# Kernel optimization log

Measured on AMD Instinct MI355X. Metric: run time of the kernel, lower is better.

The kernel has to match this reference:

```python
import jax, jax.numpy as jnp
import numpy as np

NOPE, ROPE, LORA, VDIM = 128, 64, 512, 128
H, T = 16, 2048
SCALE = 1.0 / float(np.sqrt(NOPE + ROPE))  # 192**-0.5


def setup_inputs() -> dict:
    key = jax.random.key(0)
    k1, k2, k3, k4, k5 = jax.random.split(key, 5)
    return {
        "query": jax.random.normal(k1, (T, H, NOPE + ROPE), jnp.float32),
        "k_c_normed": jax.random.normal(k2, (T, LORA), jnp.float32),
        "k_pe": jax.random.normal(k3, (T, ROPE), jnp.float32),
        "w_kv_b": jax.random.normal(k4, (LORA, H * (NOPE + VDIM)), jnp.float32) * 0.02,
        "w_uv": jax.random.normal(k5, (H, LORA, VDIM), jnp.float32) * 0.02,
    }


def reference(query, k_c_normed, k_pe, w_kv_b, w_uv):
    # Causal (fresh-token, "compute friendly") MLA path of HPUUnifiedMLAImpl.
    t = query.shape[0]
    # kv_b_proj: latent -> per-head [nope | v]; only k_nope is used for scoring
    kv_nope = (k_c_normed @ w_kv_b).reshape(t, H, NOPE + VDIM)
    k_nope = kv_nope[..., :NOPE]                                   # [T,H,128]
    # k = cat(k_nope, broadcast k_pe) -> [T,H,192]
    k = jnp.concatenate(
        [k_nope, jnp.broadcast_to(k_pe[:, None, :], (t, H, ROPE))], axis=-1)
    # causal attention scores [H,T,T]
    scores = jnp.einsum('thd,shd->hts', query, k) * SCALE
    mask = jnp.tril(jnp.ones((t, t), dtype=bool))                  # causal
    scores = jnp.where(mask[None], scores, jnp.finfo(scores.dtype).min)
    p = jax.nn.softmax(scores, axis=-1)
    # value is the latent k_c, shared across heads (v_causal_latent expand)
    out_latent = jnp.einsum('hts,sl->thl', p, k_c_normed)          # [T,H,512]
    # W_UV projects latent attn output -> full v dim
    out = jnp.einsum('thl,hlv->thv', out_latent, w_uv)             # [T,H,128]
    return out.reshape(t, H * VDIM)
```

## Files before the change

### kernel.cpp

```cpp
#include <hip/hip_runtime.h>
#include <hip/hip_bf16.h>
#include <math.h>

#define T_SEQ 2048
#define NHEAD 16
#define DQK 192
#define DNOPE 128
#define DROPE 64
#define LORA_D 512
#define VDIM 128
#define SCALE_F 0.072168783648703216f
#define KC 32

typedef short bf16x8 __attribute__((ext_vector_type(8)));
typedef float f32x4 __attribute__((ext_vector_type(4)));

static __device__ __forceinline__ unsigned short f2bf(float x) {
  union { float f; unsigned int u; } v; v.f = x;
  unsigned int r = (v.u + 0x7fff + ((v.u >> 16) & 1)) >> 16;
  return (unsigned short)r;
}

__global__ __launch_bounds__(256) void stage_all(
    const float* __restrict__ k_c, const float* __restrict__ w_kv_b,
    const float* __restrict__ w_uv, unsigned short* __restrict__ Ab,
    unsigned short* __restrict__ BkT, unsigned short* __restrict__ BvT)
{
  __shared__ float tile[32][33];
  const int bx = blockIdx.x, role = blockIdx.y;
  const int tid = threadIdx.x;
  if (role == 0) {
    int i = (bx * 256 + tid) * 4;
    float4 v = *(const float4*)(k_c + i);
    ushort4 o = {f2bf(v.x), f2bf(v.y), f2bf(v.z), f2bf(v.w)};
    *(ushort4*)(Ab + i) = o;
    return;
  }
  const int tk = tid >> 3, tc4 = (tid & 7) * 4;
  const int wr = tid >> 3, wk4 = (tid & 7) * 4;
  if (role == 1) {
    const int k0 = (bx & 15) * 32, n0 = (bx >> 4) * 32;
    int n = n0 + tc4;
    int col = n + ((n >> 7) << 7);
    float4 v = *(const float4*)&w_kv_b[(size_t)(k0 + tk) * 4096 + col];
    tile[tk][tc4 + 0] = v.x; tile[tk][tc4 + 1] = v.y;
    tile[tk][tc4 + 2] = v.z; tile[tk][tc4 + 3] = v.w;
    __syncthreads();
    ushort4 o = {f2bf(tile[wk4 + 0][wr]), f2bf(tile[wk4 + 1][wr]),
                 f2bf(tile[wk4 + 2][wr]), f2bf(tile[wk4 + 3][wr])};
    *(ushort4*)&BkT[(size_t)(n0 + wr) * LORA_D + k0 + wk4] = o;
  } else {
    const int k0 = (bx & 15) * 32, v0 = ((bx >> 4) & 3) * 32, h = bx >> 6;
    float4 v = *(const float4*)&w_uv[(size_t)h * 65536 + (size_t)(k0 + tk) * 128 + v0 + tc4];
    tile[tk][tc4 + 0] = v.x; tile[tk][tc4 + 1] = v.y;
    tile[tk][tc4 + 2] = v.z; tile[tk][tc4 + 3] = v.w;
    __syncthreads();
    ushort4 o = {f2bf(tile[wk4 + 0][wr]), f2bf(tile[wk4 + 1][wr]),
                 f2bf(tile[wk4 + 2][wr]), f2bf(tile[wk4 + 3][wr])};
    *(ushort4*)&BvT[(size_t)(h * VDIM + v0 + wr) * LORA_D + k0 + wk4] = o;
  }
}

__global__ __launch_bounds__(256) void prep_gemm(
    const unsigned short* __restrict__ A, const unsigned short* __restrict__ BkT,
    const unsigned short* __restrict__ BvT, const float* __restrict__ k_pe,
    unsigned short* __restrict__ Kb, unsigned short* __restrict__ Vt)
{
  __shared__ unsigned short SMEM[32768];
  const int m0 = blockIdx.x * 128;
  const int by = blockIdx.y;
  const int isK = (by < 16);
  const int n0 = (isK ? by : (by - 16)) * 128;
  const unsigned short* BT = isK ? BkT : BvT;
  const int tid = threadIdx.x;
  const int wid = tid >> 6, lane = tid & 63;
  const int l16 = lane & 15, quad = lane >> 4;
  const int wm = (wid >> 1) * 64, wn = (wid & 1) * 64;

  auto stage_pg = [&](int b, int k0) {
    const char* Asrc = (const char*)(A + (size_t)m0 * LORA_D + k0);
    const char* Bsrc = (const char*)(BT + (size_t)n0 * LORA_D + k0);
    char* Adst = (char*)SMEM + b * 16384;
    char* Bdst = (char*)SMEM + 32768 + b * 16384;
#pragma unroll
    for (int i = 0; i < 4; ++i) {
      int d = tid * 16 + i * 4096;
      int row = d >> 7, c = d & 127;
      int sc = c ^ ((row & 7) << 4);
      __builtin_amdgcn_global_load_lds(
          (const unsigned int*)(Asrc + (size_t)row * 1024 + sc),
          (unsigned int*)(Adst + d), 16, 0, 0);
      __builtin_amdgcn_global_load_lds(
          (const unsigned int*)(Bsrc + (size_t)row * 1024 + sc),
          (unsigned int*)(Bdst + d), 16, 0, 0);
    }
  };

  f32x4 acc[4][4];
#pragma unroll
  for (int i = 0; i < 4; ++i)
#pragma unroll
    for (int j = 0; j < 4; ++j) acc[i][j] = (f32x4){0.f, 0.f, 0.f, 0.f};

  stage_pg(0, 0);
  __syncthreads();
  for (int kc = 0; kc < 8; ++kc) {
    const int cur = kc & 1;
    if (kc < 7) stage_pg(cur ^ 1, (kc + 1) * 64);
#pragma unroll
    for (int kk = 0; kk < 2; ++kk) {
      bf16x8 af[4], bfr[4];
#pragma unroll
      for (int t = 0; t < 4; ++t) {
        int ra = wm + t * 16 + l16;
        af[t] = *(const bf16x8*)((char*)SMEM + cur * 16384 + ra * 128 +
                                 (((kk * 4 + quad) ^ (ra & 7)) << 4));
        int rb = wn + t * 16 + l16;
        bfr[t] = *(const bf16x8*)((char*)SMEM + 32768 + cur * 16384 + rb * 128 +
                                  (((kk * 4 + quad) ^ (rb & 7)) << 4));
      }
#pragma unroll
      for (int mt = 0; mt < 4; ++mt)
#pragma unroll
        for (int nt = 0; nt < 4; ++nt)
          acc[mt][nt] = __builtin_amdgcn_mfma_f32_16x16x32_bf16(af[mt], bfr[nt], acc[mt][nt], 0, 0, 0);
    }
    __syncthreads();
  }

  unsigned short* E = SMEM;
  if (isK) {
#pragma unroll
    for (int mt = 0; mt < 4; ++mt)
#pragma unroll
      for (int nt = 0; nt < 4; ++nt) {
        int ml = wm + mt * 16 + quad * 4;
        int d = wn + nt * 16 + l16;
#pragma unroll
        for (int r = 0; r < 4; ++r)
          E[(ml + r) * 136 + d] = f2bf(acc[mt][nt][r]);
      }
  } else {
#pragma unroll
    for (int mt = 0; mt < 4; ++mt)
#pragma unroll
      for (int nt = 0; nt < 4; ++nt) {
        int ml = wm + mt * 16 + quad * 4;
        int nl = wn + nt * 16 + l16;
#pragma unroll
        for (int r = 0; r < 4; ++r)
          E[nl * 136 + ml + r] = f2bf(acc[mt][nt][r]);
      }
  }
  __syncthreads();

  if (isK) {
    const int h = by;
#pragma unroll
    for (int i = 0; i < 8; ++i) {
      int idx = (i * 256 + tid) * 8;
      int row = idx >> 7, col = idx & 127;
      uint4 v = *(const uint4*)&E[row * 136 + col];
      *(uint4*)&Kb[(size_t)h * (T_SEQ * DQK) + (size_t)(m0 + row) * DQK + col] = v;
    }
    for (int e = tid; e < 128 * 16; e += 256) {
      int row = e >> 4, c4 = (e & 15) * 4;
      float4 v = *(const float4*)&k_pe[(size_t)(m0 + row) * DROPE + c4];
      ushort4 o = {f2bf(v.x), f2bf(v.y), f2bf(v.z), f2bf(v.w)};
      *(ushort4*)&Kb[(size_t)h * (T_SEQ * DQK) + (size_t)(m0 + row) * DQK + DNOPE + c4] = o;
    }
  } else {
#pragma unroll
    for (int i = 0; i < 8; ++i) {
      int idx = (i * 256 + tid) * 8;
      int row = idx >> 7, col = idx & 127;
      uint4 v = *(const uint4*)&E[row * 136 + col];
      *(uint4*)&Vt[(size_t)(n0 + row) * T_SEQ + m0 + col] = v;
    }
  }
}

__global__ __launch_bounds__(256, 4) void flash_mfma(
    const float* __restrict__ Q, const unsigned short* __restrict__ K,
    const unsigned short* __restrict__ Vt, float* __restrict__ outp,
    float* __restrict__ Opart, float* __restrict__ Lpart, int adaptive)
{
  __shared__ unsigned short SM[2 * KC * DQK];
  __shared__ unsigned short Vsm[2 * VDIM * KC];
  const int id = blockIdx.x;
  const int h = ((id & 7) << 1) | ((id >> 3) & 1);
  int q0, c0, c1, slot, direct;
  if (adaptive) {
    const int b = 79 - (id >> 4);
    int j, sp, s;
    if (b < 8)       { j = b;               sp = 0;            s = 1; }
    else if (b < 24) { j = 8 + (b - 8) / 2; sp = (b - 8) % 2;  s = 2; }
    else if (b < 48) { j = 16 + (b - 24) / 3; sp = (b - 24) % 3; s = 3; }
    else             { j = 24 + (b - 48) / 4; sp = (b - 48) % 4; s = 4; }
    q0 = j * 64;
    const int n = 2 * j + 2;
    c0 = (n * sp) / s;
    c1 = (n * (sp + 1)) / s;
    direct = (s == 1);
    slot = h * 72 + (b - 8);
  } else {
    q0 = (31 - (id >> 4)) * 64;
    c0 = 0; c1 = q0 / KC + 2; direct = 1; slot = 0;
  }
  const int tid = threadIdx.x;
  const int wid = tid >> 6;
  const int lane = tid & 63;
  const int l16 = lane & 15;
  const int quad = lane >> 4;
  const int myrow = q0 + wid * 16 + quad * 4;
  const int qrow  = q0 + wid * 16 + l16;
  const int nch = c1 - c0;

  const unsigned short* Kh = K + (size_t)h * T_SEQ * DQK;
  const unsigned short* Vth = Vt + (size_t)h * VDIM * T_SEQ;

  int ksrc_off[3], kdst_off[3];
#pragma unroll
  for (int i = 0; i < 3; ++i) {
    int d = tid * 16 + i * 4096;
    int rho = d / 384, c = d - rho * 384;
    int rr = rho & 15, hi = rho >> 4;
    int g = 8 * (rr >> 2) + 2 * (rr & 3) + hi;
    ksrc_off[i] = g * 384 + (c ^ ((rho & 7) << 4));
    kdst_off[i] = d;
  }
  size_t vsrc_off[2]; int vdst_off[2];
#pragma unroll
  for (int i = 0; i < 2; ++i) {
    int d = tid * 16 + i * 4096;
    int row = d >> 6, c = d & 63;
    vsrc_off[i] = (size_t)row * (T_SEQ * 2) + (c ^ ((row & 3) << 4));
    vdst_off[i] = d;
  }

  auto stage = [&](int buf, int s0) {
    const char* Kc = (const char*)Kh + (size_t)s0 * 384;
    char* Kd = (char*)&SM[buf * (KC * DQK)];
#pragma unroll
    for (int i = 0; i < 3; ++i)
      __builtin_amdgcn_global_load_lds(
          (const unsigned int*)(Kc + ksrc_off[i]),
          (unsigned int*)(Kd + kdst_off[i]), 16, 0, 0);
    const char* Vc = (const char*)Vth + (size_t)s0 * 2;
    char* Vd = (char*)&Vsm[buf * (VDIM * KC)];
#pragma unroll
    for (int i = 0; i < 2; ++i)
      __builtin_amdgcn_global_load_lds(
          (const unsigned int*)(Vc + vsrc_off[i]),
          (unsigned int*)(Vd + vdst_off[i]), 16, 0, 0);
  };

  for (int e = tid; e < 64 * 48; e += 256) {
    int row = e / 48, col = (e % 48) * 4;
    float4 q4 = *(const float4*)&Q[(size_t)(q0 + row) * (NHEAD * DQK) + h * DQK + col];
    ushort4 qp = {f2bf(q4.x), f2bf(q4.y), f2bf(q4.z), f2bf(q4.w)};
    *(ushort4*)&SM[row * DQK + col] = qp;
  }
  __syncthreads();
  bf16x8 qf[6];
#pragma unroll
  for (int ks = 0; ks < 6; ++ks)
    qf[ks] = *(const bf16x8*)&SM[(wid * 16 + l16) * DQK + ks * 32 + quad * 8];
  __syncthreads();
  stage(0, c0 * KC);
  __syncthreads();

  f32x4 oacc[8];
#pragma unroll
  for (int i = 0; i < 8; ++i) oacc[i] = (f32x4){0.f, 0.f, 0.f, 0.f};
  float lsum = 0.f;

  for (int ck = 0; ck < nch; ++ck) {
    const int cur = ck & 1;
    const int s0 = (c0 + ck) * KC;
    if (ck + 1 < nch) stage(cur ^ 1, s0 + KC);

    const char* Kbase = (const char*)&SM[cur * (KC * DQK)];
    f32x4 sacc0 = (f32x4){0.f, 0.f, 0.f, 0.f};
    f32x4 sacc1 = (f32x4){0.f, 0.f, 0.f, 0.f};
    __builtin_amdgcn_s_setprio(1);
#pragma unroll
    for (int ks = 0; ks < 6; ++ks) {
      int c = ks * 64 + quad * 16;
      int r0 = l16, r1 = 16 + l16;
      bf16x8 kf0 = *(const bf16x8*)(Kbase + r0 * 384 + (c ^ ((r0 & 7) << 4)));
      bf16x8 kf1 = *(const bf16x8*)(Kbase + r1 * 384 + (c ^ ((r1 & 7) << 4)));
      sacc0 = __builtin_amdgcn_mfma_f32_16x16x32_bf16(kf0, qf[ks], sacc0, 0, 0, 0);
      sacc1 = __builtin_amdgcn_mfma_f32_16x16x32_bf16(kf1, qf[ks], sacc1, 0, 0, 0);
    }
    __builtin_amdgcn_s_setprio(0);

    union { unsigned int u[4]; bf16x8 v; } pw;
#pragma unroll
    for (int r = 0; r < 4; ++r) {
      int kva = s0 + quad * 8 + 2 * r;
      float e0 = (kva <= qrow)     ? __expf(sacc0[r] * SCALE_F) : 0.f;
      float e1 = (kva + 1 <= qrow) ? __expf(sacc1[r] * SCALE_F) : 0.f;
      lsum += e0 + e1;
      asm("v_cvt_pk_bf16_f32 %0, %1, %2" : "=v"(pw.u[r]) : "v"(e0), "v"(e1));
    }
    bf16x8 pf = pw.v;

    const char* Vbase = (const char*)&Vsm[cur * (VDIM * KC)];
    __builtin_amdgcn_s_setprio(1);
#pragma unroll
    for (int nt = 0; nt < 8; ++nt) {
      int vrow = nt * 16 + l16;
      bf16x8 vf = *(const bf16x8*)(Vbase + vrow * 64 + ((quad * 16) ^ ((vrow & 3) << 4)));
      oacc[nt] = __builtin_amdgcn_mfma_f32_16x16x32_bf16(pf, vf, oacc[nt], 0, 0, 0);
    }
    __builtin_amdgcn_s_setprio(0);

    __syncthreads();
  }

  lsum += __shfl_xor(lsum, 16);
  lsum += __shfl_xor(lsum, 32);
  float rowsum[4];
#pragma unroll
  for (int r = 0; r < 4; ++r) rowsum[r] = __shfl(lsum, quad * 4 + r, 64);

  if (direct) {
    float inv[4];
#pragma unroll
    for (int r = 0; r < 4; ++r) inv[r] = 1.f / rowsum[r];
#pragma unroll
    for (int nt = 0; nt < 8; ++nt)
#pragma unroll
      for (int r = 0; r < 4; ++r)
        outp[(size_t)(myrow + r) * (NHEAD * VDIM) + h * VDIM + nt * 16 + l16] =
            oacc[nt][r] * inv[r];
  } else {
    const int rbase = wid * 16 + quad * 4;
#pragma unroll
    for (int nt = 0; nt < 8; ++nt)
#pragma unroll
      for (int r = 0; r < 4; ++r)
        Opart[(size_t)slot * 8192 + (rbase + r) * 128 + nt * 16 + l16] =
            oacc[nt][r];
    if (l16 == 0)
#pragma unroll
      for (int r = 0; r < 4; ++r)
        Lpart[slot * 64 + rbase + r] = rowsum[r];
  }
}

__global__ __launch_bounds__(256) void reduce_out(
    const float* __restrict__ Opart, const float* __restrict__ Lpart,
    float* __restrict__ outp)
{
  const int t = blockIdx.x;
  const int h = t & 15;
  const int j = 8 + (t >> 4);
  int s, b0;
  if (j < 16)      { s = 2; b0 = 8 + (j - 8) * 2; }
  else if (j < 24) { s = 3; b0 = 24 + (j - 16) * 3; }
  else             { s = 4; b0 = 48 + (j - 24) * 4; }
  const int slot = h * 72 + (b0 - 8);
  const int q0 = j * 64;
  const int tid = threadIdx.x;
#pragma unroll
  for (int i = 0; i < 8; ++i) {
    const int f4 = tid + i * 256;
    const int row = f4 >> 5, cc = f4 & 31;
    float ax = 0.f, ay = 0.f, az = 0.f, aw = 0.f, l = 0.f;
    for (int k = 0; k < s; ++k) {
      float4 v = ((const float4*)Opart)[(size_t)(slot + k) * 2048 + f4];
      ax += v.x; ay += v.y; az += v.z; aw += v.w;
      l += Lpart[(slot + k) * 64 + row];
    }
    const float inv = 1.f / l;
    float4 o = {ax * inv, ay * inv, az * inv, aw * inv};
    ((float4*)outp)[(size_t)(q0 + row) * 512 + h * 32 + cc] = o;
  }
}

extern "C" void kernel_launch(void* const* d_in, const int* in_sizes, int n_in,
                              void* d_out, int out_size, void* d_ws, size_t ws_size,
                              hipStream_t stream) {
  const float* query  = (const float*)d_in[0];
  const float* k_c    = (const float*)d_in[1];
  const float* k_pe   = (const float*)d_in[2];
  const float* w_kv_b = (const float*)d_in[3];
  const float* w_uv   = (const float*)d_in[4];
  float* outp = (float*)d_out;

  unsigned short* Kb  = (unsigned short*)d_ws;
  unsigned short* Vt  = Kb + (size_t)NHEAD * T_SEQ * DQK;
  unsigned short* Ab  = Vt + (size_t)NHEAD * VDIM * T_SEQ;
  unsigned short* BkT = Ab + (size_t)T_SEQ * LORA_D;
  unsigned short* BvT = BkT + (size_t)2048 * LORA_D;
  float* Opart = (float*)(BvT + (size_t)2048 * LORA_D);
  float* Lpart = Opart + (size_t)16 * 72 * 64 * 128;
  const size_t need =
      (size_t)((char*)(Lpart + (size_t)16 * 72 * 64) - (char*)d_ws);
  const int adaptive = (ws_size >= need) ? 1 : 0;

  stage_all<<<dim3(1024, 3), 256, 0, stream>>>(k_c, w_kv_b, w_uv, Ab, BkT, BvT);
  prep_gemm<<<dim3(16, 32), 256, 0, stream>>>(Ab, BkT, BvT, k_pe, Kb, Vt);
  flash_mfma<<<adaptive ? 1280 : 512, 256, 0, stream>>>(query, Kb, Vt, outp,
                                                        Opart, Lpart, adaptive);
  if (adaptive)
    reduce_out<<<384, 256, 0, stream>>>(Opart, Lpart, outp);
}
```

Baseline: 167.0 us.

## Fuse split-KV reduction into flash kernel via atomic last-block counter

Removes the separate reduce_out launch. Each split block now bumps a per-(head, query-tile) atomic counter, and the last block to finish sums the partial outputs and row sums and writes the normalized result. This drops one kernel launch and lets the reduction overlap with other blocks still running. In exchange it adds a threadfence, two barriers, a memset launch for the counters, and serialized reduction work on the last-arriving block.

```diff
diff --git a/kernel.cpp b/kernel.cpp
--- a/kernel.cpp
+++ b/kernel.cpp
@@ -183,13 +183,15 @@
 __global__ __launch_bounds__(256, 4) void flash_mfma(
     const float* __restrict__ Q, const unsigned short* __restrict__ K,
     const unsigned short* __restrict__ Vt, float* __restrict__ outp,
-    float* __restrict__ Opart, float* __restrict__ Lpart, int adaptive)
+    float* __restrict__ Opart, float* __restrict__ Lpart,
+    int* __restrict__ Cnt, int adaptive)
 {
   __shared__ unsigned short SM[2 * KC * DQK];
   __shared__ unsigned short Vsm[2 * VDIM * KC];
   const int id = blockIdx.x;
   const int h = ((id & 7) << 1) | ((id >> 3) & 1);
   int q0, c0, c1, slot, direct;
+  int jj = 0, spW = 0, sW = 1;
   if (adaptive) {
     const int b = 79 - (id >> 4);
     int j, sp, s;
@@ -203,6 +205,7 @@
     c1 = (n * (sp + 1)) / s;
     direct = (s == 1);
     slot = h * 72 + (b - 8);
+    jj = j; spW = sp; sW = s;
   } else {
     q0 = (31 - (id >> 4)) * 64;
     c0 = 0; c1 = q0 / KC + 2; direct = 1; slot = 0;
@@ -347,36 +350,36 @@
 #pragma unroll
       for (int r = 0; r < 4; ++r)
         Lpart[slot * 64 + rbase + r] = rowsum[r];
-  }
-}
-
-__global__ __launch_bounds__(256) void reduce_out(
-    const float* __restrict__ Opart, const float* __restrict__ Lpart,
-    float* __restrict__ outp)
-{
-  const int t = blockIdx.x;
-  const int h = t & 15;
-  const int j = 8 + (t >> 4);
-  int s, b0;
-  if (j < 16)      { s = 2; b0 = 8 + (j - 8) * 2; }
-  else if (j < 24) { s = 3; b0 = 24 + (j - 16) * 3; }
-  else             { s = 4; b0 = 48 + (j - 24) * 4; }
-  const int slot = h * 72 + (b0 - 8);
-  const int q0 = j * 64;
-  const int tid = threadIdx.x;
-#pragma unroll
-  for (int i = 0; i < 8; ++i) {
-    const int f4 = tid + i * 256;
-    const int row = f4 >> 5, cc = f4 & 31;
-    float ax = 0.f, ay = 0.f, az = 0.f, aw = 0.f, l = 0.f;
-    for (int k = 0; k < s; ++k) {
-      float4 v = ((const float4*)Opart)[(size_t)(slot + k) * 2048 + f4];
-      ax += v.x; ay += v.y; az += v.z; aw += v.w;
-      l += Lpart[(slot + k) * 64 + row];
-    }
-    const float inv = 1.f / l;
-    float4 o = {ax * inv, ay * inv, az * inv, aw * inv};
-    ((float4*)outp)[(size_t)(q0 + row) * 512 + h * 32 + cc] = o;
+
+    __threadfence();
+    __syncthreads();
+    volatile int* lf = (volatile int*)&SM[0];
+    if (tid == 0) {
+      const int gid = h * 24 + (jj - 8);
+      int old = atomicAdd(&Cnt[gid], 1);
+      int last = (old == sW - 1) ? 1 : 0;
+      if (last) Cnt[gid] = 0;
+      *lf = last;
+    }
+    __syncthreads();
+    if (*lf) {
+      __threadfence();
+      const int slot0 = slot - spW;
+#pragma unroll
+      for (int i = 0; i < 8; ++i) {
+        const int f4 = tid + i * 256;
+        const int row = f4 >> 5, cc = f4 & 31;
+        float ax = 0.f, ay = 0.f, az = 0.f, aw = 0.f, l = 0.f;
+        for (int k = 0; k < sW; ++k) {
+          float4 v = ((const float4*)Opart)[(size_t)(slot0 + k) * 2048 + f4];
+          ax += v.x; ay += v.y; az += v.z; aw += v.w;
+          l += Lpart[(slot0 + k) * 64 + row];
+        }
+        const float inv = 1.f / l;
+        float4 o = {ax * inv, ay * inv, az * inv, aw * inv};
+        ((float4*)outp)[(size_t)(q0 + row) * 512 + h * 32 + cc] = o;
+      }
+    }
   }
 }
 
@@ -397,14 +400,14 @@
   unsigned short* BvT = BkT + (size_t)2048 * LORA_D;
   float* Opart = (float*)(BvT + (size_t)2048 * LORA_D);
   float* Lpart = Opart + (size_t)16 * 72 * 64 * 128;
-  const size_t need =
-      (size_t)((char*)(Lpart + (size_t)16 * 72 * 64) - (char*)d_ws);
+  int*   Cnt   = (int*)(Lpart + (size_t)16 * 72 * 64);
+  const size_t need = (size_t)((char*)(Cnt + 384) - (char*)d_ws);
   const int adaptive = (ws_size >= need) ? 1 : 0;
 
   stage_all<<<dim3(1024, 3), 256, 0, stream>>>(k_c, w_kv_b, w_uv, Ab, BkT, BvT);
   prep_gemm<<<dim3(16, 32), 256, 0, stream>>>(Ab, BkT, BvT, k_pe, Kb, Vt);
+  if (adaptive)
+    hipMemsetAsync(Cnt, 0, 384 * sizeof(int), stream);
   flash_mfma<<<adaptive ? 1280 : 512, 256, 0, stream>>>(query, Kb, Vt, outp,
-                                                        Opart, Lpart, adaptive);
-  if (adaptive)
-    reduce_out<<<384, 256, 0, stream>>>(Opart, Lpart, outp);
+                                                        Opart, Lpart, Cnt, adaptive);
 }
```

Result: slower. 355.3 us (+112.7%).
